# Optimization experiments

Measured on AMD Instinct MI355X. Metric: run time of the kernel, lower is better.

## Reference

```python
import jax, jax.numpy as jnp
import numpy as np

EPS = 1e-8  # matches torch cosine_similarity eps


def setup_inputs() -> dict:
    key = jax.random.key(0)
    ks = jax.random.split(key, 8)
    B, D_IN, H, L = 256, 256, 256, 100000
    G = 5 * H  # (N_GATES + 1) * hidden_dim
    s_in = 1.0 / np.sqrt(D_IN)
    s_h = 1.0 / np.sqrt(H)
    return {
        "x_t": jax.random.normal(ks[0], (B, D_IN), jnp.float32),
        "h": jax.random.normal(ks[1], (B, H), jnp.float32),
        "c": jax.random.normal(ks[2], (B, H), jnp.float32),
        "W_i2h": jax.random.normal(ks[3], (G, D_IN), jnp.float32) * s_in,
        "b_i2h": jnp.zeros((G,), jnp.float32),
        "W_h2h": jax.random.normal(ks[4], (G, H), jnp.float32) * s_h,
        "b_h2h": jnp.zeros((G,), jnp.float32),
        "keys": jax.random.normal(ks[5], (L, D_IN), jnp.float32),
        "vals": jax.random.normal(ks[6], (L, H), jnp.float32),
    }


def _dnd_get_memory(q, keys, vals):
    # cosine similarity of each query against every stored key -> [B, L]
    qn = q / jnp.maximum(jnp.linalg.norm(q, axis=-1, keepdims=True), EPS)
    kn = keys / jnp.maximum(jnp.linalg.norm(keys, axis=-1, keepdims=True), EPS)
    sims = jnp.einsum("bd,ld->bl", qn, kn)
    w = jax.nn.softmax(sims, axis=-1)          # softmax-weighted aggregation
    return jnp.einsum("bl,lh->bh", w, vals)    # [B, H]


def reference(x_t, h, c, W_i2h, b_i2h, W_h2h, b_h2h, keys, vals):
    H = h.shape[1]
    preact = (x_t @ W_i2h.T + b_i2h) + (h @ W_h2h.T + b_h2h)   # [B, 5H]
    gates = jax.nn.sigmoid(preact[:, : 4 * H])
    f_t = gates[:, :H]
    i_t = gates[:, H:2 * H]
    o_t = gates[:, 2 * H:3 * H]
    r_t = gates[:, 3 * H:4 * H]
    c_t_new = jnp.tanh(preact[:, 4 * H:])
    c_t = f_t * c + i_t * c_t_new
    m_t = jnp.tanh(_dnd_get_memory(x_t, keys, vals))
    c_t = c_t + r_t * m_t
    h_t = o_t * jnp.tanh(c_t)
    return (h_t, c_t)
```

## Files before the change

### kernel.cpp

```cpp
#include <hip/hip_runtime.h>
#include <stdint.h>

typedef float f4_t __attribute__((ext_vector_type(4)));
typedef __bf16 bf8_t __attribute__((ext_vector_type(8)));
typedef unsigned short us4_t __attribute__((ext_vector_type(4)));
typedef unsigned short us8_t __attribute__((ext_vector_type(8)));

static __device__ __forceinline__ unsigned short fbf(float f) {
    __bf16 b = (__bf16)f;
    return *(unsigned short*)&b;
}
static __device__ __forceinline__ float bf2f(unsigned short u) {
    union { uint32_t u; float f; } v; v.u = ((uint32_t)u) << 16;
    return v.f;
}
static __device__ __forceinline__ f4_t mfma16(bf8_t a, bf8_t b, f4_t c) {
    return __builtin_amdgcn_mfma_f32_16x16x32_bf16(a, b, c, 0, 0, 0);
}
static __device__ __forceinline__ float sigf(float x) {
    return 1.0f / (1.0f + __expf(-x));
}

__global__ __launch_bounds__(256) void k_convert(
    const float* __restrict__ x, const float* __restrict__ h,
    const float* __restrict__ W1, const float* __restrict__ W2,
    unsigned short* __restrict__ qn, unsigned short* __restrict__ xb,
    unsigned short* __restrict__ hb, unsigned short* __restrict__ w1b,
    unsigned short* __restrict__ w2b)
{
    __shared__ float sred[4];
    int bid = blockIdx.x, t = threadIdx.x;
    if (bid < 256) {
        float v = x[bid * 256 + t];
        float ss = v * v;
        #pragma unroll
        for (int m = 1; m < 64; m <<= 1) ss += __shfl_xor(ss, m, 64);
        if ((t & 63) == 0) sred[t >> 6] = ss;
        __syncthreads();
        float tot = sred[0] + sred[1] + sred[2] + sred[3];
        float rn = 1.0f / fmaxf(sqrtf(tot), 1e-8f);
        xb[bid * 256 + t] = fbf(v);
        qn[bid * 256 + t] = fbf(v * rn);
    } else if (bid < 512) {
        int b = bid - 256;
        hb[b * 256 + t] = fbf(h[b * 256 + t]);
    } else {
        int i0 = (bid - 512) * 256 + t;
        for (int i = i0; i < 1280 * 256; i += 512 * 256) {
            w1b[i] = fbf(W1[i]);
            w2b[i] = fbf(W2[i]);
        }
    }
}

__global__ __launch_bounds__(256) void k_gates(
    const unsigned short* __restrict__ xb, const unsigned short* __restrict__ hb,
    const unsigned short* __restrict__ w1b, const unsigned short* __restrict__ w2b,
    const float* __restrict__ b1, const float* __restrict__ b2,
    float* __restrict__ pre)
{
    int bb = (blockIdx.x & 3) * 64;
    int gb = (blockIdx.x >> 2) * 64;
    int t = threadIdx.x, w = t >> 6, lane = t & 63;
    int l15 = lane & 15, q8 = (lane >> 4) * 8, q4 = (lane >> 4) * 4;
    int arow = bb + w * 16 + l15;

    f4_t acc[4] = {};
    #pragma unroll
    for (int ks = 0; ks < 8; ++ks) {
        bf8_t a = *(const bf8_t*)&xb[arow * 256 + ks * 32 + q8];
        #pragma unroll
        for (int gc = 0; gc < 4; ++gc) {
            bf8_t bf = *(const bf8_t*)&w1b[(gb + gc * 16 + l15) * 256 + ks * 32 + q8];
            acc[gc] = mfma16(a, bf, acc[gc]);
        }
    }
    #pragma unroll
    for (int ks = 0; ks < 8; ++ks) {
        bf8_t a = *(const bf8_t*)&hb[arow * 256 + ks * 32 + q8];
        #pragma unroll
        for (int gc = 0; gc < 4; ++gc) {
            bf8_t bf = *(const bf8_t*)&w2b[(gb + gc * 16 + l15) * 256 + ks * 32 + q8];
            acc[gc] = mfma16(a, bf, acc[gc]);
        }
    }
    #pragma unroll
    for (int gc = 0; gc < 4; ++gc) {
        int g = gb + gc * 16 + l15;
        float bias = b1[g] + b2[g];
        #pragma unroll
        for (int r = 0; r < 4; ++r) {
            int b = bb + w * 16 + q4 + r;
            pre[b * 1280 + g] = acc[gc][r] + bias;
        }
    }
}

__global__ __launch_bounds__(512, 1) void k_dnd(
    const float* __restrict__ keys, const float* __restrict__ vals,
    const unsigned short* __restrict__ qn,
    unsigned short* __restrict__ opart, float* __restrict__ dpart,
    int L, int CH)
{
    __shared__ __align__(16) char smem[147456];
    unsigned short* Pl = (unsigned short*)(smem + 131072);

    const int t = threadIdx.x;
    const int w = t >> 6, lane = t & 63;
    const int l15 = lane & 15;
    const int q8 = (lane >> 4) * 8, q4 = (lane >> 4) * 4;

    const int bid = blockIdx.x;
    const int bhalf = (bid >> 3) & 1;
    const int chunk = (bid & 7) | ((bid >> 4) << 3);
    const int base = chunk * CH;
    int nkeys = L - base;
    if (nkeys > CH) nkeys = CH;
    if (nkeys < 0) nkeys = 0;
    const int nt = (nkeys + 63) >> 6;

    const int kr = t >> 3;
    const int j8 = t & 7;

    bf8_t qa[8];
    #pragma unroll
    for (int ks = 0; ks < 8; ++ks)
        qa[ks] = *(const bf8_t*)&qn[(bhalf * 128 + w * 16 + l15) * 256 + ks * 32 + q8];

    f4_t o[16] = {};
    float den[4] = {};
    f4_t kst[8], vst[8];

    auto issueK = [&](int tt) {
        int row = base + tt * 64 + kr;
        if (row >= L) row = L - 1;
        const float* src = keys + (size_t)row * 256;
        #pragma unroll
        for (int m = 0; m < 8; ++m) kst[m] = *(const f4_t*)(src + m * 32 + j8 * 4);
    };
    auto issueV = [&](int tt) {
        #pragma unroll
        for (int r = 0; r < 8; ++r) {
            int row = base + tt * 64 + w * 8 + r;
            if (row >= L) row = L - 1;
            vst[r] = *(const f4_t*)&vals[(size_t)row * 256 + lane * 4];
        }
    };
    auto stage = [&](char* kb, char* vb) {
        float ss = 0.f;
        #pragma unroll
        for (int m = 0; m < 8; ++m)
            ss += kst[m][0]*kst[m][0] + kst[m][1]*kst[m][1]
                + kst[m][2]*kst[m][2] + kst[m][3]*kst[m][3];
        ss += __shfl_xor(ss, 1, 64);
        ss += __shfl_xor(ss, 2, 64);
        ss += __shfl_xor(ss, 4, 64);
        float rn = 1.0f / fmaxf(sqrtf(ss), 1e-8f);
        unsigned short* K = (unsigned short*)kb;
        #pragma unroll
        for (int m = 0; m < 8; ++m) {
            us4_t uv;
            uv[0] = fbf(kst[m][0]*rn); uv[1] = fbf(kst[m][1]*rn);
            uv[2] = fbf(kst[m][2]*rn); uv[3] = fbf(kst[m][3]*rn);
            int el = m * 32 + j8 * 4;
            *(us4_t*)&K[kr * 256 + (el ^ ((kr & 7) * 8))] = uv;
        }
        unsigned short* V = (unsigned short*)vb;
        #pragma unroll
        for (int j = 0; j < 4; ++j) {
            int hh = 4 * lane + j;
            int f = ((hh >> 2) ^ hh) & 7;
            us8_t uv;
            #pragma unroll
            for (int r = 0; r < 8; ++r) uv[r] = fbf(vst[r][j]);
            *(us8_t*)&V[hh * 64 + ((w * 8) ^ (f * 8))] = uv;
        }
    };

    if (nt > 0) {
        issueK(0); issueV(0);
        asm volatile("s_waitcnt vmcnt(0)" ::: "memory");
        stage(smem, smem + 65536);
        if (nt > 1) { issueK(1); issueV(1); __builtin_amdgcn_sched_barrier(0); }
        asm volatile("s_waitcnt lgkmcnt(0)\n\ts_barrier" ::: "memory");

        for (int tt = 0; tt < nt; ++tt) {
            const int cur = tt & 1;
            const unsigned short* Kl = (const unsigned short*)(smem + cur * 32768);
            const unsigned short* Vl = (const unsigned short*)(smem + 65536 + cur * 32768);

            f4_t s[4] = {};
            __builtin_amdgcn_s_setprio(1);
            #pragma unroll
            for (int lc = 0; lc < 4; ++lc) {
                int l = lc * 16 + l15;
                int sw = (l & 7) * 8;
                #pragma unroll
                for (int ks = 0; ks < 8; ++ks) {
                    bf8_t kf = *(const bf8_t*)&Kl[l * 256 + ((ks * 32 + q8) ^ sw)];
                    s[lc] = mfma16(qa[ks], kf, s[lc]);
                }
            }
            __builtin_amdgcn_s_setprio(0);

            #pragma unroll
            for (int lc = 0; lc < 4; ++lc) {
                int l = lc * 16 + l15;
                bool valid = (tt * 64 + l) < nkeys;
                #pragma unroll
                for (int r = 0; r < 4; ++r) {
                    float p = valid ? __expf(s[lc][r] - 1.0f) : 0.0f;
                    den[r] += p;
                    int br = w * 16 + q4 + r;
                    Pl[br * 64 + (l ^ ((br & 7) * 8))] = fbf(p);
                }
            }

            {
                int brow = w * 16 + l15;
                int swp = (brow & 7) * 8;
                bf8_t pa0 = *(const bf8_t*)&Pl[brow * 64 + (q8 ^ swp)];
                bf8_t pa1 = *(const bf8_t*)&Pl[brow * 64 + ((32 + q8) ^ swp)];
                __builtin_amdgcn_s_setprio(1);
                #pragma unroll
                for (int hc = 0; hc < 16; ++hc) {
                    int hh = hc * 16 + l15;
                    int fr = (((hh >> 2) ^ hh) & 7) * 8;
                    bf8_t vf0 = *(const bf8_t*)&Vl[hh * 64 + (q8 ^ fr)];
                    bf8_t vf1 = *(const bf8_t*)&Vl[hh * 64 + ((32 + q8) ^ fr)];
                    o[hc] = mfma16(pa0, vf0, o[hc]);
                    o[hc] = mfma16(pa1, vf1, o[hc]);
                }
                __builtin_amdgcn_s_setprio(0);
            }

            if (tt + 1 < nt) {
                asm volatile("s_waitcnt vmcnt(0)" ::: "memory");
                stage(smem + (cur ^ 1) * 32768, smem + 65536 + (cur ^ 1) * 32768);
                if (tt + 2 < nt) {
                    issueK(tt + 2); issueV(tt + 2);
                    __builtin_amdgcn_sched_barrier(0);
                }
                asm volatile("s_waitcnt lgkmcnt(0)\n\ts_barrier" ::: "memory");
            }
        }
    }

    __syncthreads();
    unsigned short* Ol = (unsigned short*)smem;
    #pragma unroll
    for (int hc = 0; hc < 16; ++hc)
        #pragma unroll
        for (int r = 0; r < 4; ++r)
            Ol[(w * 16 + q4 + r) * 256 + hc * 16 + l15] = fbf(o[hc][r]);
    __syncthreads();
    {
        size_t ob = (size_t)(chunk * 2 + bhalf) * 32768;
        #pragma unroll
        for (int it = 0; it < 8; ++it) {
            int off = it * 4096 + t * 8;
            *(us8_t*)&opart[ob + off] = *(const us8_t*)&Ol[off];
        }
    }
    #pragma unroll
    for (int r = 0; r < 4; ++r) {
        float d = den[r];
        #pragma unroll
        for (int m = 1; m < 16; m <<= 1) d += __shfl_xor(d, m, 64);
        if (l15 == 0)
            dpart[chunk * 256 + bhalf * 128 + w * 16 + q4 + r] = d;
    }
}

__global__ __launch_bounds__(256) void k_reduce(
    const unsigned short* __restrict__ opart, const float* __restrict__ dpart,
    const float* __restrict__ pre, const float* __restrict__ c_in,
    float* __restrict__ out)
{
    __shared__ float sred[4];
    int b = blockIdx.x, t = threadIdx.x;

    float ds = (t < 128) ? dpart[t * 256 + b] : 0.0f;
    #pragma unroll
    for (int m = 1; m < 64; m <<= 1) ds += __shfl_xor(ds, m, 64);
    if ((t & 63) == 0) sred[t >> 6] = ds;
    __syncthreads();
    float dtot = fmaxf(sred[0] + sred[1] + sred[2] + sred[3], 1e-30f);

    int bh = b >> 7, br = b & 127;
    float n0 = 0.f, n1 = 0.f, n2 = 0.f, n3 = 0.f;
    for (int ck = 0; ck < 128; ck += 4) {
        n0 += bf2f(opart[(size_t)((ck + 0) * 2 + bh) * 32768 + br * 256 + t]);
        n1 += bf2f(opart[(size_t)((ck + 1) * 2 + bh) * 32768 + br * 256 + t]);
        n2 += bf2f(opart[(size_t)((ck + 2) * 2 + bh) * 32768 + br * 256 + t]);
        n3 += bf2f(opart[(size_t)((ck + 3) * 2 + bh) * 32768 + br * 256 + t]);
    }
    float num = (n0 + n1) + (n2 + n3);

    float m = tanhf(num / dtot);
    const float* p = pre + b * 1280;
    float fg = sigf(p[t]);
    float ig = sigf(p[256 + t]);
    float og = sigf(p[512 + t]);
    float rg = sigf(p[768 + t]);
    float cn = tanhf(p[1024 + t]);
    float co = c_in[b * 256 + t];
    float ct = fg * co + ig * cn + rg * m;
    float ht = og * tanhf(ct);
    out[b * 256 + t] = ht;
    out[65536 + b * 256 + t] = ct;
}

extern "C" void kernel_launch(void* const* d_in, const int* in_sizes, int n_in,
                              void* d_out, int out_size, void* d_ws, size_t ws_size,
                              hipStream_t stream)
{
    const float* x    = (const float*)d_in[0];
    const float* h    = (const float*)d_in[1];
    const float* c    = (const float*)d_in[2];
    const float* W1   = (const float*)d_in[3];
    const float* b1   = (const float*)d_in[4];
    const float* W2   = (const float*)d_in[5];
    const float* b2   = (const float*)d_in[6];
    const float* keys = (const float*)d_in[7];
    const float* vals = (const float*)d_in[8];
    int L = in_sizes[7] / 256;

    int TILES = (L + 128 * 64 - 1) / (128 * 64);
    int CH = TILES * 64;

    char* ws = (char*)d_ws;
    unsigned short* qn    = (unsigned short*)(ws + 0);
    unsigned short* xb    = (unsigned short*)(ws + 131072);
    unsigned short* hb    = (unsigned short*)(ws + 262144);
    unsigned short* w1b   = (unsigned short*)(ws + 393216);
    unsigned short* w2b   = (unsigned short*)(ws + 1048576);
    float*          pre   = (float*)(ws + 1703936);
    float*          dpart = (float*)(ws + 3014656);
    unsigned short* opart = (unsigned short*)(ws + 3145728);

    k_convert<<<dim3(1024), dim3(256), 0, stream>>>(x, h, W1, W2, qn, xb, hb, w1b, w2b);
    k_gates<<<dim3(80), dim3(256), 0, stream>>>(xb, hb, w1b, w2b, b1, b2, pre);
    k_dnd<<<dim3(256), dim3(512), 0, stream>>>(keys, vals, qn, opart, dpart, L, CH);
    k_reduce<<<dim3(256), dim3(256), 0, stream>>>(opart, dpart, pre, c, (float*)d_out);

    (void)n_in; (void)out_size; (void)ws_size;
}
```

Baseline: 117.9 us.

## Restructure DND kernel to split hidden dim and stage via global_load_lds

The DND kernel now splits work across blocks by halves of the value hidden dimension instead of batch halves, so each block handles all 256 queries against 32-key tiles. Raw fp32 keys and values go straight into LDS through global_load_lds, then a convert pass normalizes and bf16-packs them into double-buffered swizzled tiles. Shared memory is cut so two blocks can share a CU (launch bounds 512,2), and the reduce kernel's indexing changes to the new partial layout. Each key tile is now loaded and its similarities computed by both hidden-half blocks, which doubles key traffic and QK MFMA work. There are also extra barriers per tile and more register pressure from the two query sets.

```diff
diff --git a/kernel.cpp b/kernel.cpp
--- a/kernel.cpp
+++ b/kernel.cpp
@@ -19,6 +19,11 @@
 }
 static __device__ __forceinline__ float sigf(float x) {
     return 1.0f / (1.0f + __expf(-x));
+}
+static __device__ __forceinline__ void gload_lds16(const void* g, void* l) {
+    __builtin_amdgcn_global_load_lds(
+        (const __attribute__((address_space(1))) void*)g,
+        (__attribute__((address_space(3))) void*)l, 16, 0, 0);
 }
 
 __global__ __launch_bounds__(256) void k_convert(
@@ -96,14 +101,14 @@
     }
 }
 
-__global__ __launch_bounds__(512, 1) void k_dnd(
+__global__ __launch_bounds__(512, 2) void k_dnd(
     const float* __restrict__ keys, const float* __restrict__ vals,
     const unsigned short* __restrict__ qn,
     unsigned short* __restrict__ opart, float* __restrict__ dpart,
     int L, int CH)
 {
-    __shared__ __align__(16) char smem[147456];
-    unsigned short* Pl = (unsigned short*)(smem + 131072);
+    __shared__ __align__(16) char smem[114688];
+    unsigned short* Pl = (unsigned short*)(smem + 98304);
 
     const int t = threadIdx.x;
     const int w = t >> 6, lane = t & 63;
@@ -111,164 +116,181 @@
     const int q8 = (lane >> 4) * 8, q4 = (lane >> 4) * 4;
 
     const int bid = blockIdx.x;
-    const int bhalf = (bid >> 3) & 1;
+    const int hhalf = (bid >> 3) & 1;
     const int chunk = (bid & 7) | ((bid >> 4) << 3);
     const int base = chunk * CH;
     int nkeys = L - base;
     if (nkeys > CH) nkeys = CH;
     if (nkeys < 0) nkeys = 0;
-    const int nt = (nkeys + 63) >> 6;
-
-    const int kr = t >> 3;
-    const int j8 = t & 7;
-
-    bf8_t qa[8];
-    #pragma unroll
-    for (int ks = 0; ks < 8; ++ks)
-        qa[ks] = *(const bf8_t*)&qn[(bhalf * 128 + w * 16 + l15) * 256 + ks * 32 + q8];
-
-    f4_t o[16] = {};
-    float den[4] = {};
-    f4_t kst[8], vst[8];
-
-    auto issueK = [&](int tt) {
-        int row = base + tt * 64 + kr;
-        if (row >= L) row = L - 1;
-        const float* src = keys + (size_t)row * 256;
-        #pragma unroll
-        for (int m = 0; m < 8; ++m) kst[m] = *(const f4_t*)(src + m * 32 + j8 * 4);
+    const int nt = (nkeys + 31) >> 5;
+
+    bf8_t qa[2][8];
+    #pragma unroll
+    for (int bt = 0; bt < 2; ++bt)
+        #pragma unroll
+        for (int ks = 0; ks < 8; ++ks)
+            qa[bt][ks] = *(const bf8_t*)&qn[(w * 32 + bt * 16 + l15) * 256 + ks * 32 + q8];
+
+    f4_t o[2][8] = {};
+    float den[2][4] = {};
+
+    auto issueRaw = [&](int tt) {
+        #pragma unroll
+        for (int i = 0; i < 4; ++i) {
+            int lrow = 4 * w + i;
+            int row = base + tt * 32 + lrow;
+            if (row >= L) row = L - 1;
+            gload_lds16(keys + (size_t)row * 256 + lane * 4,
+                        smem + lrow * 1024);
+        }
+        #pragma unroll
+        for (int c = 0; c < 2; ++c) {
+            int lrow = 4 * w + 2 * c;
+            int row = base + tt * 32 + lrow + (lane >> 5);
+            if (row >= L) row = L - 1;
+            gload_lds16(vals + (size_t)row * 256 + hhalf * 128 + (lane & 31) * 4,
+                        smem + 32768 + lrow * 512);
+        }
     };
-    auto issueV = [&](int tt) {
-        #pragma unroll
-        for (int r = 0; r < 8; ++r) {
-            int row = base + tt * 64 + w * 8 + r;
-            if (row >= L) row = L - 1;
-            vst[r] = *(const f4_t*)&vals[(size_t)row * 256 + lane * 4];
+
+    auto convert = [&](int buf) {
+        unsigned short* Kb = (unsigned short*)(smem + 49152 + buf * 16384);
+        unsigned short* Vb = (unsigned short*)(smem + 81920 + buf * 8192);
+        const float* Kraw = (const float*)smem;
+        const float* Vraw = (const float*)(smem + 32768);
+        {
+            int row = t >> 4, c16 = (t & 15) * 16;
+            f4_t a0 = *(const f4_t*)&Kraw[row * 256 + c16];
+            f4_t a1 = *(const f4_t*)&Kraw[row * 256 + c16 + 4];
+            f4_t a2 = *(const f4_t*)&Kraw[row * 256 + c16 + 8];
+            f4_t a3 = *(const f4_t*)&Kraw[row * 256 + c16 + 12];
+            float ss = a0[0]*a0[0]+a0[1]*a0[1]+a0[2]*a0[2]+a0[3]*a0[3]
+                     + a1[0]*a1[0]+a1[1]*a1[1]+a1[2]*a1[2]+a1[3]*a1[3]
+                     + a2[0]*a2[0]+a2[1]*a2[1]+a2[2]*a2[2]+a2[3]*a2[3]
+                     + a3[0]*a3[0]+a3[1]*a3[1]+a3[2]*a3[2]+a3[3]*a3[3];
+            ss += __shfl_xor(ss, 1, 64);
+            ss += __shfl_xor(ss, 2, 64);
+            ss += __shfl_xor(ss, 4, 64);
+            ss += __shfl_xor(ss, 8, 64);
+            float rn = 1.0f / fmaxf(sqrtf(ss), 1e-8f);
+            int sw = (row & 7) * 8;
+            us8_t u0, u1;
+            u0[0]=fbf(a0[0]*rn); u0[1]=fbf(a0[1]*rn); u0[2]=fbf(a0[2]*rn); u0[3]=fbf(a0[3]*rn);
+            u0[4]=fbf(a1[0]*rn); u0[5]=fbf(a1[1]*rn); u0[6]=fbf(a1[2]*rn); u0[7]=fbf(a1[3]*rn);
+            u1[0]=fbf(a2[0]*rn); u1[1]=fbf(a2[1]*rn); u1[2]=fbf(a2[2]*rn); u1[3]=fbf(a2[3]*rn);
+            u1[4]=fbf(a3[0]*rn); u1[5]=fbf(a3[1]*rn); u1[6]=fbf(a3[2]*rn); u1[7]=fbf(a3[3]*rn);
+            *(us8_t*)&Kb[row * 256 + (c16 ^ sw)]       = u0;
+            *(us8_t*)&Kb[row * 256 + ((c16 + 8) ^ sw)] = u1;
+        }
+        {
+            int hh = t & 127, oct = t >> 7;
+            us8_t uv;
+            #pragma unroll
+            for (int r = 0; r < 8; ++r)
+                uv[r] = fbf(Vraw[(oct * 8 + r) * 128 + hh]);
+            int slot = (((hh & 15) * 4 + oct) ^ ((hh & 14) >> 1));
+            *(us8_t*)&Vb[(hh >> 4) * 512 + slot * 8] = uv;
         }
     };
-    auto stage = [&](char* kb, char* vb) {
-        float ss = 0.f;
-        #pragma unroll
-        for (int m = 0; m < 8; ++m)
-            ss += kst[m][0]*kst[m][0] + kst[m][1]*kst[m][1]
-                + kst[m][2]*kst[m][2] + kst[m][3]*kst[m][3];
-        ss += __shfl_xor(ss, 1, 64);
-        ss += __shfl_xor(ss, 2, 64);
-        ss += __shfl_xor(ss, 4, 64);
-        float rn = 1.0f / fmaxf(sqrtf(ss), 1e-8f);
-        unsigned short* K = (unsigned short*)kb;
-        #pragma unroll
-        for (int m = 0; m < 8; ++m) {
-            us4_t uv;
-            uv[0] = fbf(kst[m][0]*rn); uv[1] = fbf(kst[m][1]*rn);
-            uv[2] = fbf(kst[m][2]*rn); uv[3] = fbf(kst[m][3]*rn);
-            int el = m * 32 + j8 * 4;
-            *(us4_t*)&K[kr * 256 + (el ^ ((kr & 7) * 8))] = uv;
-        }
-        unsigned short* V = (unsigned short*)vb;
-        #pragma unroll
-        for (int j = 0; j < 4; ++j) {
-            int hh = 4 * lane + j;
-            int f = ((hh >> 2) ^ hh) & 7;
-            us8_t uv;
-            #pragma unroll
-            for (int r = 0; r < 8; ++r) uv[r] = fbf(vst[r][j]);
-            *(us8_t*)&V[hh * 64 + ((w * 8) ^ (f * 8))] = uv;
-        }
-    };
 
     if (nt > 0) {
-        issueK(0); issueV(0);
+        issueRaw(0);
         asm volatile("s_waitcnt vmcnt(0)" ::: "memory");
-        stage(smem, smem + 65536);
-        if (nt > 1) { issueK(1); issueV(1); __builtin_amdgcn_sched_barrier(0); }
+        __builtin_amdgcn_s_barrier();
+        convert(0);
         asm volatile("s_waitcnt lgkmcnt(0)\n\ts_barrier" ::: "memory");
+        if (nt > 1) issueRaw(1);
 
         for (int tt = 0; tt < nt; ++tt) {
             const int cur = tt & 1;
-            const unsigned short* Kl = (const unsigned short*)(smem + cur * 32768);
-            const unsigned short* Vl = (const unsigned short*)(smem + 65536 + cur * 32768);
-
-            f4_t s[4] = {};
+            const unsigned short* Kb = (const unsigned short*)(smem + 49152 + cur * 16384);
+            const unsigned short* Vb = (const unsigned short*)(smem + 81920 + cur * 8192);
+
+            f4_t s[2][2] = {};
             __builtin_amdgcn_s_setprio(1);
             #pragma unroll
-            for (int lc = 0; lc < 4; ++lc) {
+            for (int lc = 0; lc < 2; ++lc) {
                 int l = lc * 16 + l15;
                 int sw = (l & 7) * 8;
                 #pragma unroll
                 for (int ks = 0; ks < 8; ++ks) {
-                    bf8_t kf = *(const bf8_t*)&Kl[l * 256 + ((ks * 32 + q8) ^ sw)];
-                    s[lc] = mfma16(qa[ks], kf, s[lc]);
+                    bf8_t kf = *(const bf8_t*)&Kb[l * 256 + ((ks * 32 + q8) ^ sw)];
+                    s[0][lc] = mfma16(qa[0][ks], kf, s[0][lc]);
+                    s[1][lc] = mfma16(qa[1][ks], kf, s[1][lc]);
                 }
             }
             __builtin_amdgcn_s_setprio(0);
 
             #pragma unroll
-            for (int lc = 0; lc < 4; ++lc) {
+            for (int lc = 0; lc < 2; ++lc) {
                 int l = lc * 16 + l15;
-                bool valid = (tt * 64 + l) < nkeys;
+                bool valid = (tt * 32 + l) < nkeys;
                 #pragma unroll
-                for (int r = 0; r < 4; ++r) {
-                    float p = valid ? __expf(s[lc][r] - 1.0f) : 0.0f;
-                    den[r] += p;
-                    int br = w * 16 + q4 + r;
-                    Pl[br * 64 + (l ^ ((br & 7) * 8))] = fbf(p);
-                }
+                for (int bt = 0; bt < 2; ++bt)
+                    #pragma unroll
+                    for (int r = 0; r < 4; ++r) {
+                        float p = valid ? __expf(s[bt][lc][r] - 1.0f) : 0.0f;
+                        den[bt][r] += p;
+                        int b = w * 32 + bt * 16 + q4 + r;
+                        Pl[b * 32 + l] = fbf(p);
+                    }
             }
 
             {
-                int brow = w * 16 + l15;
-                int swp = (brow & 7) * 8;
-                bf8_t pa0 = *(const bf8_t*)&Pl[brow * 64 + (q8 ^ swp)];
-                bf8_t pa1 = *(const bf8_t*)&Pl[brow * 64 + ((32 + q8) ^ swp)];
+                bf8_t pa0 = *(const bf8_t*)&Pl[(w * 32 + l15) * 32 + q8];
+                bf8_t pa1 = *(const bf8_t*)&Pl[(w * 32 + 16 + l15) * 32 + q8];
                 __builtin_amdgcn_s_setprio(1);
                 #pragma unroll
-                for (int hc = 0; hc < 16; ++hc) {
+                for (int hc = 0; hc < 8; ++hc) {
                     int hh = hc * 16 + l15;
-                    int fr = (((hh >> 2) ^ hh) & 7) * 8;
-                    bf8_t vf0 = *(const bf8_t*)&Vl[hh * 64 + (q8 ^ fr)];
-                    bf8_t vf1 = *(const bf8_t*)&Vl[hh * 64 + ((32 + q8) ^ fr)];
-                    o[hc] = mfma16(pa0, vf0, o[hc]);
-                    o[hc] = mfma16(pa1, vf1, o[hc]);
+                    int slot = (((hh & 15) * 4 + (q8 >> 3)) ^ ((hh & 14) >> 1));
+                    bf8_t vf = *(const bf8_t*)&Vb[hc * 512 + slot * 8];
+                    o[0][hc] = mfma16(pa0, vf, o[0][hc]);
+                    o[1][hc] = mfma16(pa1, vf, o[1][hc]);
                 }
                 __builtin_amdgcn_s_setprio(0);
             }
 
             if (tt + 1 < nt) {
                 asm volatile("s_waitcnt vmcnt(0)" ::: "memory");
-                stage(smem + (cur ^ 1) * 32768, smem + 65536 + (cur ^ 1) * 32768);
-                if (tt + 2 < nt) {
-                    issueK(tt + 2); issueV(tt + 2);
-                    __builtin_amdgcn_sched_barrier(0);
-                }
+                __builtin_amdgcn_s_barrier();
+                convert(cur ^ 1);
                 asm volatile("s_waitcnt lgkmcnt(0)\n\ts_barrier" ::: "memory");
-            }
-        }
-    }
-
+                if (tt + 2 < nt) issueRaw(tt + 2);
+            }
+        }
+    }
+
+    asm volatile("s_waitcnt vmcnt(0)" ::: "memory");
     __syncthreads();
     unsigned short* Ol = (unsigned short*)smem;
     #pragma unroll
-    for (int hc = 0; hc < 16; ++hc)
-        #pragma unroll
-        for (int r = 0; r < 4; ++r)
-            Ol[(w * 16 + q4 + r) * 256 + hc * 16 + l15] = fbf(o[hc][r]);
+    for (int bt = 0; bt < 2; ++bt)
+        #pragma unroll
+        for (int hc = 0; hc < 8; ++hc)
+            #pragma unroll
+            for (int r = 0; r < 4; ++r)
+                Ol[(w * 32 + bt * 16 + q4 + r) * 128 + hc * 16 + l15] = fbf(o[bt][hc][r]);
     __syncthreads();
     {
-        size_t ob = (size_t)(chunk * 2 + bhalf) * 32768;
+        size_t ob = (size_t)(chunk * 2 + hhalf) * 32768;
         #pragma unroll
         for (int it = 0; it < 8; ++it) {
             int off = it * 4096 + t * 8;
             *(us8_t*)&opart[ob + off] = *(const us8_t*)&Ol[off];
         }
     }
-    #pragma unroll
-    for (int r = 0; r < 4; ++r) {
-        float d = den[r];
-        #pragma unroll
-        for (int m = 1; m < 16; m <<= 1) d += __shfl_xor(d, m, 64);
-        if (l15 == 0)
-            dpart[chunk * 256 + bhalf * 128 + w * 16 + q4 + r] = d;
+    if (hhalf == 0) {
+        #pragma unroll
+        for (int bt = 0; bt < 2; ++bt)
+            #pragma unroll
+            for (int r = 0; r < 4; ++r) {
+                float d = den[bt][r];
+                #pragma unroll
+                for (int m = 1; m < 16; m <<= 1) d += __shfl_xor(d, m, 64);
+                if (l15 == 0)
+                    dpart[chunk * 256 + w * 32 + bt * 16 + q4 + r] = d;
+            }
     }
 }
 
@@ -287,13 +309,14 @@
     __syncthreads();
     float dtot = fmaxf(sred[0] + sred[1] + sred[2] + sred[3], 1e-30f);
 
-    int bh = b >> 7, br = b & 127;
+    int bh = t >> 7, hcol = t & 127;
+    size_t sb = (size_t)b * 128 + hcol + (size_t)bh * 32768;
     float n0 = 0.f, n1 = 0.f, n2 = 0.f, n3 = 0.f;
     for (int ck = 0; ck < 128; ck += 4) {
-        n0 += bf2f(opart[(size_t)((ck + 0) * 2 + bh) * 32768 + br * 256 + t]);
-        n1 += bf2f(opart[(size_t)((ck + 1) * 2 + bh) * 32768 + br * 256 + t]);
-        n2 += bf2f(opart[(size_t)((ck + 2) * 2 + bh) * 32768 + br * 256 + t]);
-        n3 += bf2f(opart[(size_t)((ck + 3) * 2 + bh) * 32768 + br * 256 + t]);
+        n0 += bf2f(opart[(size_t)(ck + 0) * 65536 + sb]);
+        n1 += bf2f(opart[(size_t)(ck + 1) * 65536 + sb]);
+        n2 += bf2f(opart[(size_t)(ck + 2) * 65536 + sb]);
+        n3 += bf2f(opart[(size_t)(ck + 3) * 65536 + sb]);
     }
     float num = (n0 + n1) + (n2 + n3);
 
@@ -326,8 +349,8 @@
     const float* vals = (const float*)d_in[8];
     int L = in_sizes[7] / 256;
 
-    int TILES = (L + 128 * 64 - 1) / (128 * 64);
-    int CH = TILES * 64;
+    int TILES = (L + 128 * 32 - 1) / (128 * 32);
+    int CH = TILES * 32;
 
     char* ws = (char*)d_ws;
     unsigned short* qn    = (unsigned short*)(ws + 0);
```

After: 99.82 us. -15.4%, faster.
